# Kernel optimization log

Measured on AMD Instinct MI355X. Metric: run time of the kernel, lower is better.

Reference implementation:

```python
import jax, jax.numpy as jnp
import numpy as np

N_NODES = 50000
N_EDGES = 400000
DIMS = [128, 1024, 512, 256, 64, 1]  # ConvGraphNet layer widths


def setup_inputs() -> dict:
    key = jax.random.key(0)
    ks = jax.random.split(key, 2 + 2 * 5)
    inp = {}
    inp["x"] = jax.random.normal(ks[0], (N_NODES, DIMS[0]), dtype=jnp.float32)
    inp["edge_index"] = jax.random.randint(ks[1], (2, N_EDGES), 0, N_NODES, dtype=jnp.int32)
    for i in range(5):
        fan_in, fan_out = DIMS[i], DIMS[i + 1]
        scale = (1.0 / np.sqrt(fan_in)).astype(np.float32)
        inp[f"W{i+1}"] = jax.random.normal(ks[2 + 2 * i], (fan_in, fan_out), dtype=jnp.float32) * scale
        inp[f"b{i+1}"] = jax.random.normal(ks[3 + 2 * i], (fan_out,), dtype=jnp.float32) * 0.01
    return inp


def _gcn_forward(x, edge_index, params):
    # PyG GCNConv: add self-loops, symmetric deg^{-1/2} normalization,
    # h = x @ W, out[dst] += norm * h[src], + bias. ReLU after each layer.
    src, dst = edge_index[0], edge_index[1]
    loop = jnp.arange(N_NODES, dtype=src.dtype)
    src_f = jnp.concatenate([src, loop])  # [E + N]
    dst_f = jnp.concatenate([dst, loop])
    deg = jax.ops.segment_sum(jnp.ones_like(src_f, dtype=x.dtype), dst_f, num_segments=N_NODES)
    dinv = jnp.where(deg > 0, jax.lax.rsqrt(jnp.maximum(deg, 1e-12)), 0.0).astype(x.dtype)
    norm = (dinv[src_f] * dinv[dst_f])[:, None]  # [E + N, 1]
    for W, b in params:
        h = x @ W                      # [N, F_out] dense GEMM (small)
        msg = h[src_f] * norm          # gather + scale  [E+N, F_out]
        agg = jax.ops.segment_sum(msg, dst_f, num_segments=N_NODES)  # scatter-add
        x = jax.nn.relu(agg + b)
    return x


def reference(x, edge_index, W1, b1, W2, b2, W3, b3, W4, b4, W5, b5):
    params = [(W1, b1), (W2, b2), (W3, b3), (W4, b4), (W5, b5)]
    return _gcn_forward(x, edge_index, params)
```

## Files before the change

kernel.cpp:

```cpp
#include <hip/hip_runtime.h>
#include <hip/hip_bf16.h>

#define N_NODES_DIM0 128

typedef unsigned short u16;
typedef unsigned int u32;
typedef __attribute__((ext_vector_type(8))) short short8;
typedef __attribute__((ext_vector_type(4))) float f32x4;

__device__ __forceinline__ float bf2f(u16 h) { return __uint_as_float((u32)h << 16); }
__device__ __forceinline__ u16 f2bf(float f) {
    u32 u = __float_as_uint(f);
    u32 r = (u + 0x7FFFu + ((u >> 16) & 1u)) >> 16;
    return (u16)r;
}

__device__ __forceinline__ void gl2lds16(const u16* g, u16* lds_base) {
    __builtin_amdgcn_global_load_lds(
        (const __attribute__((address_space(1))) u32*)g,
        (__attribute__((address_space(3))) u32*)lds_base, 16, 0, 0);
}


__global__ void hist_kernel(const int* __restrict__ dst, int* __restrict__ cnt, int e) {
    int i = blockIdx.x * blockDim.x + threadIdx.x;
    if (i < e) atomicAdd(&cnt[dst[i]], 1);
}

__global__ void alloc_kernel(const int* __restrict__ cnt, int* __restrict__ row_start,
                             float* __restrict__ dinv, int* __restrict__ cursor, int n) {
    int i = blockIdx.x * blockDim.x + threadIdx.x;
    int lane = threadIdx.x & 63;
    int v = (i < n) ? cnt[i] : 0;
    int s = v;
#pragma unroll
    for (int off = 1; off < 64; off <<= 1) {
        int x = __shfl_up(s, off, 64);
        if (lane >= off) s += x;
    }
    int total = __shfl(s, 63, 64);
    int base = 0;
    if (lane == 0) base = atomicAdd(cursor, total);
    base = __shfl(base, 0, 64);
    if (i < n) {
        row_start[i] = base + s - v;
        dinv[i] = rsqrtf((float)v + 1.0f);
    }
}

__global__ void fill_kernel(const int* __restrict__ src, const int* __restrict__ dst,
                            int* __restrict__ row_start, int* __restrict__ csr_src, int e) {
    int i = blockIdx.x * blockDim.x + threadIdx.x;
    if (i < e) {
        int d = dst[i];
        int pos = atomicAdd(&row_start[d], 1);
        csr_src[pos] = src[i];
    }
}

__global__ __launch_bounds__(256) void prep_kernel(
    const float* __restrict__ W0, const float* __restrict__ W1,
    const float* __restrict__ W2, const float* __restrict__ W3, u16* __restrict__ Wt,
    const float* __restrict__ x, const float* __restrict__ dinv,
    u16* __restrict__ Y, int N) {
    int bid = blockIdx.x;
    if (bid < 784) {
        __shared__ float tile[32][33];
        const float* W; u16* out; int K, F, kb, nb;
        if (bid < 128)      { W = W0; out = Wt;          K = 128;  F = 1024; kb = bid & 3;  nb = bid >> 2; }
        else if (bid < 640) { int l = bid - 128; W = W1; out = Wt + 131072; K = 1024; F = 512; kb = l & 31; nb = l >> 5; }
        else if (bid < 768) { int l = bid - 640; W = W2; out = Wt + 655360; K = 512;  F = 256; kb = l & 15; nb = l >> 4; }
        else                { int l = bid - 768; W = W3; out = Wt + 786432; K = 256;  F = 64;  kb = l & 7;  nb = l >> 3; }
        int k0 = kb * 32, n0 = nb * 32;
        int tx = threadIdx.x & 31, ty = threadIdx.x >> 5;
#pragma unroll
        for (int i = 0; i < 4; ++i) {
            int k = ty + i * 8;
            tile[k][tx] = W[(size_t)(k0 + k) * F + n0 + tx];
        }
        __syncthreads();
#pragma unroll
        for (int i = 0; i < 4; ++i) {
            int n = ty + i * 8;
            out[(size_t)(n0 + n) * K + k0 + tx] = f2bf(tile[tx][n]);
        }
    } else {
        int gid = (bid - 784) * 256 + threadIdx.x;
        int node = gid >> 5;
        int c4 = (gid & 31) * 4;
        if (node >= N) return;
        float dv = dinv[node];
        float4 v = *reinterpret_cast<const float4*>(x + (size_t)node * 128 + c4);
        ushort4 r;
        r.x = f2bf(dv * v.x); r.y = f2bf(dv * v.y);
        r.z = f2bf(dv * v.z); r.w = f2bf(dv * v.w);
        *reinterpret_cast<ushort4*>(Y + (size_t)node * 128 + c4) = r;
    }
}

__device__ __forceinline__ void add8v(float* acc, short8 v) {
#pragma unroll
    for (int w = 0; w < 8; ++w) acc[w] += bf2f((u16)v[w]);
}
__device__ __forceinline__ void add16p(float* acc, const u16* p) {
    short8 a = *reinterpret_cast<const short8*>(p);
    short8 b = *reinterpret_cast<const short8*>(p + 8);
    add8v(acc, a); add8v(acc + 8, b);
}

__device__ __forceinline__ void gather_sum16(float* acc, const u16* __restrict__ base,
                                             const int* __restrict__ csr_src,
                                             int beg, int end, int stride, int ch) {
    int e = beg;
    int nfull = (end - beg) >> 3;
    if (nfull > 0) {
        int i0 = csr_src[e],     i1 = csr_src[e + 1], i2 = csr_src[e + 2], i3 = csr_src[e + 3];
        int i4 = csr_src[e + 4], i5 = csr_src[e + 5], i6 = csr_src[e + 6], i7 = csr_src[e + 7];
        for (int b = 0; b < nfull; ++b) {
            const u16* p0 = base + (size_t)i0 * stride + ch;
            const u16* p1 = base + (size_t)i1 * stride + ch;
            const u16* p2 = base + (size_t)i2 * stride + ch;
            const u16* p3 = base + (size_t)i3 * stride + ch;
            const u16* p4 = base + (size_t)i4 * stride + ch;
            const u16* p5 = base + (size_t)i5 * stride + ch;
            const u16* p6 = base + (size_t)i6 * stride + ch;
            const u16* p7 = base + (size_t)i7 * stride + ch;
            short8 a0 = *reinterpret_cast<const short8*>(p0), b0 = *reinterpret_cast<const short8*>(p0 + 8);
            short8 a1 = *reinterpret_cast<const short8*>(p1), b1 = *reinterpret_cast<const short8*>(p1 + 8);
            short8 a2 = *reinterpret_cast<const short8*>(p2), b2 = *reinterpret_cast<const short8*>(p2 + 8);
            short8 a3 = *reinterpret_cast<const short8*>(p3), b3 = *reinterpret_cast<const short8*>(p3 + 8);
            short8 a4 = *reinterpret_cast<const short8*>(p4), b4 = *reinterpret_cast<const short8*>(p4 + 8);
            short8 a5 = *reinterpret_cast<const short8*>(p5), b5 = *reinterpret_cast<const short8*>(p5 + 8);
            short8 a6 = *reinterpret_cast<const short8*>(p6), b6 = *reinterpret_cast<const short8*>(p6 + 8);
            short8 a7 = *reinterpret_cast<const short8*>(p7), b7 = *reinterpret_cast<const short8*>(p7 + 8);
            e += 8;
            int ep = (e + 8 <= end) ? e : beg;
            i0 = csr_src[ep];     i1 = csr_src[ep + 1]; i2 = csr_src[ep + 2]; i3 = csr_src[ep + 3];
            i4 = csr_src[ep + 4]; i5 = csr_src[ep + 5]; i6 = csr_src[ep + 6]; i7 = csr_src[ep + 7];
            __builtin_amdgcn_sched_barrier(0);
            add8v(acc, a0); add8v(acc + 8, b0);
            add8v(acc, a1); add8v(acc + 8, b1);
            add8v(acc, a2); add8v(acc + 8, b2);
            add8v(acc, a3); add8v(acc + 8, b3);
            add8v(acc, a4); add8v(acc + 8, b4);
            add8v(acc, a5); add8v(acc + 8, b5);
            add8v(acc, a6); add8v(acc + 8, b6);
            add8v(acc, a7); add8v(acc + 8, b7);
        }
    }
    for (; e + 4 <= end; e += 4) {
        const u16* p0 = base + (size_t)csr_src[e]     * stride + ch;
        const u16* p1 = base + (size_t)csr_src[e + 1] * stride + ch;
        const u16* p2 = base + (size_t)csr_src[e + 2] * stride + ch;
        const u16* p3 = base + (size_t)csr_src[e + 3] * stride + ch;
        short8 a0 = *reinterpret_cast<const short8*>(p0), b0 = *reinterpret_cast<const short8*>(p0 + 8);
        short8 a1 = *reinterpret_cast<const short8*>(p1), b1 = *reinterpret_cast<const short8*>(p1 + 8);
        short8 a2 = *reinterpret_cast<const short8*>(p2), b2 = *reinterpret_cast<const short8*>(p2 + 8);
        short8 a3 = *reinterpret_cast<const short8*>(p3), b3 = *reinterpret_cast<const short8*>(p3 + 8);
        __builtin_amdgcn_sched_barrier(0);
        add8v(acc, a0); add8v(acc + 8, b0);
        add8v(acc, a1); add8v(acc + 8, b1);
        add8v(acc, a2); add8v(acc + 8, b2);
        add8v(acc, a3); add8v(acc + 8, b3);
    }
    for (; e < end; ++e) {
        const u16* p = base + (size_t)csr_src[e] * stride + ch;
        short8 a = *reinterpret_cast<const short8*>(p), b = *reinterpret_cast<const short8*>(p + 8);
        add8v(acc, a); add8v(acc + 8, b);
    }
}

__global__ __launch_bounds__(256, 4) void agg_pre_kernel(
        const int* __restrict__ row_end, const int* __restrict__ cnt,
        const int* __restrict__ csr_src,
        const u16* __restrict__ Y, const float* __restrict__ dinv,
        u16* __restrict__ Z, int N) {
    int gid = blockIdx.x * blockDim.x + threadIdx.x;
    int node = gid >> 3;
    int ch = (gid & 7) * 16;
    if (node >= N) return;
    float acc[16] = {};
    add16p(acc, Y + (size_t)node * 128 + ch);
    int end = row_end[node], beg = end - cnt[node];
    gather_sum16(acc, Y, csr_src, beg, end, 128, ch);
    float dv = dinv[node];
    short8 r0, r1;
#pragma unroll
    for (int w = 0; w < 8; ++w) {
        r0[w] = (short)f2bf(dv * acc[w]);
        r1[w] = (short)f2bf(dv * acc[8 + w]);
    }
    *reinterpret_cast<short8*>(Z + (size_t)node * 128 + ch) = r0;
    *reinterpret_cast<short8*>(Z + (size_t)node * 128 + ch + 8) = r1;
}

template <int BN, int TPB, int EPI>
__global__ __launch_bounds__(TPB) void gemm_mfma_kernel(
    const u16* __restrict__ X, const u16* __restrict__ Wt,
    const float* __restrict__ dinv, const float* __restrict__ bias,
    u16* __restrict__ Out, int N, int K, int F, int lgnx) {
    constexpr int BM = 128, BK = 64;
    constexpr int RA = (BM * 8) / TPB;
    constexpr int RB = (BN * 8) / TPB;
    constexpr int WAVES = TPB / 64;
    constexpr int WAVES_N = (BN >= 64) ? (BN / 64) : 1;
    constexpr int WAVES_M = WAVES / WAVES_N;
    constexpr int WM = BM / WAVES_M;
    constexpr int WN = BN / WAVES_N;
    constexpr int NI = WM / 16;
    constexpr int NJ = WN / 16;
    __shared__ u16 As[BM * BK];
    __shared__ u16 Bs[BN * BK];

    const int t = threadIdx.x;
    const int wave = t >> 6;
    const int lane = t & 63;
    const int m16 = lane & 15;
    const int quad = lane >> 4;

    const int id = blockIdx.x;
    const int wi = id & ((8 << lgnx) - 1);
    const int g  = id >> (3 + lgnx);
    const int rb = g * 8 + (wi & 7);
    const int cb = wi >> 3;
    const int row0 = rb * BM;
    const int col0 = cb * BN;
    if (row0 >= N) return;

    const int wm = (wave / WAVES_N) * WM;
    const int wn = (wave % WAVES_N) * WN;

    const u16* aSrc[RA];
    u16* aDst[RA];
#pragma unroll
    for (int rr = 0; rr < RA; ++rr) {
        int c = rr * TPB + t;
        int r = c >> 3;
        int q = (c ^ r) & 7;
        int grow = row0 + r;
        if (grow >= N) grow = 0;
        aSrc[rr] = X + (size_t)grow * K + q * 8;
        aDst[rr] = &As[(size_t)(rr * TPB + wave * 64) * 8];
    }
    const u16* bSrc[RB];
    u16* bDst[RB];
#pragma unroll
    for (int rr = 0; rr < RB; ++rr) {
        int c = rr * TPB + t;
        int r = c >> 3;
        int q = (c ^ r) & 7;
        bSrc[rr] = Wt + (size_t)(col0 + r) * K + q * 8;
        bDst[rr] = &Bs[(size_t)(rr * TPB + wave * 64) * 8];
    }

    u32 aOff[NI][2], bOff[NJ][2];
#pragma unroll
    for (int i = 0; i < NI; ++i)
#pragma unroll
        for (int h = 0; h < 2; ++h) {
            int row = wm + i * 16 + m16;
            int qg = h * 4 + quad;
            aOff[i][h] = (u32)(((row << 3) | ((qg ^ row) & 7)) * 16);
        }
#pragma unroll
    for (int j = 0; j < NJ; ++j)
#pragma unroll
        for (int h = 0; h < 2; ++h) {
            int row = wn + j * 16 + m16;
            int qg = h * 4 + quad;
            bOff[j][h] = (u32)(((row << 3) | ((qg ^ row) & 7)) * 16);
        }
    const char* AsB = reinterpret_cast<const char*>(As);
    const char* BsB = reinterpret_cast<const char*>(Bs);

    f32x4 acc[NI][NJ] = {};

    for (int k0 = 0; k0 < K; k0 += BK) {
#pragma unroll
        for (int rr = 0; rr < RA; ++rr) {
            gl2lds16(aSrc[rr], aDst[rr]);
            aSrc[rr] += BK;
        }
#pragma unroll
        for (int rr = 0; rr < RB; ++rr) {
            gl2lds16(bSrc[rr], bDst[rr]);
            bSrc[rr] += BK;
        }
        __syncthreads();

#pragma unroll
        for (int h = 0; h < 2; ++h) {
            short8 af[NI], bf[NJ];
#pragma unroll
            for (int i = 0; i < NI; ++i)
                af[i] = *reinterpret_cast<const short8*>(AsB + aOff[i][h]);
#pragma unroll
            for (int j = 0; j < NJ; ++j)
                bf[j] = *reinterpret_cast<const short8*>(BsB + bOff[j][h]);
#pragma unroll
            for (int i = 0; i < NI; ++i)
#pragma unroll
                for (int j = 0; j < NJ; ++j)
                    acc[i][j] = __builtin_amdgcn_mfma_f32_16x16x32_bf16(af[i], bf[j], acc[i][j], 0, 0, 0);
        }
        __syncthreads();
    }

#pragma unroll
    for (int i = 0; i < NI; ++i) {
#pragma unroll
        for (int r = 0; r < 4; ++r) {
            int grow = row0 + wm + i * 16 + quad * 4 + r;
            if (grow >= N) continue;
            float dv = (EPI == 0) ? dinv[grow] : 0.f;
#pragma unroll
            for (int j = 0; j < NJ; ++j) {
                int gcol = col0 + wn + j * 16 + m16;
                float v = acc[i][j][r];
                if (EPI == 0) v = dv * v;
                else          v = fmaxf(v + bias[gcol], 0.f);
                Out[(size_t)grow * F + gcol] = f2bf(v);
            }
        }
    }
}

__global__ __launch_bounds__(256, 4) void agg_post_kernel(
        const int* __restrict__ row_end, const int* __restrict__ cnt,
        const int* __restrict__ csr_src,
        const u16* __restrict__ Gc, const float* __restrict__ dinv,
        const float* __restrict__ bias, u16* __restrict__ XO,
        int N, int F, int lgG) {
    int gid = blockIdx.x * blockDim.x + threadIdx.x;
    int node = gid >> lgG;
    int ch = (gid & ((1 << lgG) - 1)) * 16;
    if (node >= N) return;
    float acc[16] = {};
    add16p(acc, Gc + (size_t)node * F + ch);
    int end = row_end[node], beg = end - cnt[node];
    gather_sum16(acc, Gc, csr_src, beg, end, F, ch);
    float dv = dinv[node];
    short8 r0, r1;
#pragma unroll
    for (int w = 0; w < 8; ++w) {
        r0[w] = (short)f2bf(fmaxf(fmaf(dv, acc[w], bias[ch + w]), 0.f));
        r1[w] = (short)f2bf(fmaxf(fmaf(dv, acc[8 + w], bias[ch + 8 + w]), 0.f));
    }
    *reinterpret_cast<short8*>(XO + (size_t)node * F + ch) = r0;
    *reinterpret_cast<short8*>(XO + (size_t)node * F + ch + 8) = r1;
}

__global__ __launch_bounds__(256, 4) void agg_post_l5_kernel(
        const int* __restrict__ row_end, const int* __restrict__ cnt,
        const int* __restrict__ csr_src,
        const u16* __restrict__ Gc, const float* __restrict__ dinv,
        const float* __restrict__ b4, const float* __restrict__ W5,
        float* __restrict__ g5, int N) {
    int gid = blockIdx.x * blockDim.x + threadIdx.x;
    int node = gid >> 2;
    int ch = (gid & 3) * 16;
    if (node >= N) return;
    float acc[16] = {};
    add16p(acc, Gc + (size_t)node * 64 + ch);
    int end = row_end[node], beg = end - cnt[node];
    gather_sum16(acc, Gc, csr_src, beg, end, 64, ch);
    float dv = dinv[node];
    float dot = 0.f;
#pragma unroll
    for (int w = 0; w < 16; ++w) {
        float v = fmaxf(fmaf(dv, acc[w], b4[ch + w]), 0.f);
        dot = fmaf(v, W5[ch + w], dot);
    }
#pragma unroll
    for (int off = 2; off > 0; off >>= 1) dot += __shfl_down(dot, off, 4);
    if ((gid & 3) == 0) g5[node] = dv * dot;
}

__global__ void agg5_kernel(const int* __restrict__ row_end, const int* __restrict__ cnt,
                            const int* __restrict__ csr_src,
                            const float* __restrict__ g5, const float* __restrict__ dinv,
                            const float* __restrict__ b5, float* __restrict__ out, int N) {
    int i = blockIdx.x * blockDim.x + threadIdx.x;
    if (i >= N) return;
    float acc = g5[i];
    int end = row_end[i], e = end - cnt[i];
    for (; e + 4 <= end; e += 4) {
        float a = g5[csr_src[e]];
        float b = g5[csr_src[e + 1]];
        float c = g5[csr_src[e + 2]];
        float d = g5[csr_src[e + 3]];
        acc += (a + b) + (c + d);
    }
    for (; e < end; ++e) acc += g5[csr_src[e]];
    out[i] = fmaxf(fmaf(dinv[i], acc, b5[0]), 0.f);
}


static inline size_t align_up(size_t x) { return (x + 255) & ~(size_t)255; }
static inline int round_up8(int x) { return (x + 7) & ~7; }

extern "C" void kernel_launch(void* const* d_in, const int* in_sizes, int n_in,
                              void* d_out, int out_size, void* d_ws, size_t ws_size,
                              hipStream_t stream) {
    const float* x  = (const float*)d_in[0];
    const int*   ei = (const int*)d_in[1];
    const int E = in_sizes[1] / 2;
    const int N = in_sizes[0] / N_NODES_DIM0;
    const int* src = ei;
    const int* dst = ei + E;

    const float* W[5] = {(const float*)d_in[2], (const float*)d_in[4], (const float*)d_in[6],
                         (const float*)d_in[8], (const float*)d_in[10]};
    const float* B[5] = {(const float*)d_in[3], (const float*)d_in[5], (const float*)d_in[7],
                         (const float*)d_in[9], (const float*)d_in[11]};

    const int Ks[4] = {128, 1024, 512, 256};
    const int Fs[4] = {1024, 512, 256, 64};

    char* w = (char*)d_ws;
    size_t off = 0;
    float* dinv    = (float*)(w + off); off += align_up((size_t)N * 4);
    float* g5      = (float*)(w + off); off += align_up((size_t)N * 4);
    int*   cnt     = (int*)(w + off);   off += align_up((size_t)(N + 1) * 4);
    int*   rstart  = (int*)(w + off);   off += align_up((size_t)N * 4);
    int*   csr_src = (int*)(w + off);   off += align_up((size_t)E * 4);
    u16* WtBase = (u16*)(w + off);
    u16* Wt[4];
    {
        size_t cum = 0;
        for (int l = 0; l < 4; ++l) {
            Wt[l] = WtBase + cum;
            cum += (size_t)Ks[l] * Fs[l];
        }
        off += align_up(cum * 2);
    }
    char* REG = w + off;               off += align_up((size_t)N * 512 * 2);
    u16* Y  = (u16*)REG;
    u16* Z  = (u16*)(REG + align_up((size_t)N * 128 * 2));
    u16* Gc = (u16*)REG;
    u16* XA = (u16*)(w + off);         off += align_up((size_t)N * 1024 * 2);
    u16* XB = (u16*)(w + off);         off += align_up((size_t)N * 512 * 2);
    (void)ws_size;

    hipMemsetAsync(cnt, 0, (size_t)(N + 1) * 4, stream);
    hist_kernel<<<(E + 255) / 256, 256, 0, stream>>>(dst, cnt, E);
    alloc_kernel<<<(N + 255) / 256, 256, 0, stream>>>(cnt, rstart, dinv, &cnt[N], N);
    fill_kernel<<<(E + 255) / 256, 256, 0, stream>>>(src, dst, rstart, csr_src, E);

    {
        int scale_blocks = (N * 32 + 255) / 256;
        prep_kernel<<<784 + scale_blocks, 256, 0, stream>>>(
            W[0], W[1], W[2], W[3], WtBase, x, dinv, Y, N);
    }

    const int ny = (N + 127) / 128;
    const int ny8 = round_up8(ny);

    agg_pre_kernel<<<(N * 8 + 255) / 256, 256, 0, stream>>>(rstart, cnt, csr_src, Y, dinv, Z, N);
    {
        gemm_mfma_kernel<256, 512, 1><<<ny8 * 4, 512, 0, stream>>>(Z, Wt[0], dinv, B[0], XA,
                                                                   N, 128, 1024, 2);
    }

    u16* Xin[3]  = {XA, XB, XA};
    u16* Xout[3] = {XB, XA, nullptr};
    for (int l = 1; l < 4; ++l) {
        const int K = Ks[l], F = Fs[l];
        if (F >= 256) {
            int nx = F / 256;
            int lgnx = (nx == 2) ? 1 : 0;
            gemm_mfma_kernel<256, 512, 0><<<ny8 * nx, 512, 0, stream>>>(
                Xin[l - 1], Wt[l], dinv, B[l], Gc, N, K, F, lgnx);
        } else {
            gemm_mfma_kernel<64, 256, 0><<<ny8, 256, 0, stream>>>(
                Xin[l - 1], Wt[l], dinv, B[l], Gc, N, K, F, 0);
        }
        if (l < 3) {
            int lgG = (F == 512) ? 5 : 4;
            long long tot = (long long)N << lgG;
            agg_post_kernel<<<(unsigned)((tot + 255) / 256), 256, 0, stream>>>(
                rstart, cnt, csr_src, Gc, dinv, B[l], Xout[l - 1], N, F, lgG);
        } else {
            long long tot = (long long)N << 2;
            agg_post_l5_kernel<<<(unsigned)((tot + 255) / 256), 256, 0, stream>>>(
                rstart, cnt, csr_src, Gc, dinv, B[3], W[4], g5, N);
        }
    }

    agg5_kernel<<<(N + 255) / 256, 256, 0, stream>>>(rstart, cnt, csr_src, g5, dinv, B[4],
                                                     (float*)d_out, N);
}
```

Measured before the change: 414.9 us.

## Fuse layer-2 aggregation with layer-3 GEMM using LDS-resident aggregated tile

Replaces the separate layer-2 aggregation kernel and layer-3 GEMM with one kernel. Each block gathers the 512-wide neighbor sums for 64 nodes, applies bias, ReLU and bf16 rounding into a swizzled LDS tile, then multiplies that tile by W3 with MFMA while streaming W3 chunks into LDS. This removes the round trip of the 512-wide activation through global memory. In exchange it uses a large LDS footprint (about 80KB), which lowers occupancy, and the GEMM phase is small per block and re-reads W3 in every block.

```diff
diff --git a/kernel.cpp b/kernel.cpp
--- a/kernel.cpp
+++ b/kernel.cpp
@@ -170,6 +170,37 @@
     }
 }
 
+__device__ __forceinline__ void gather32(float* acc, const u16* __restrict__ base,
+                                         const int* __restrict__ csr_src,
+                                         int beg, int end, int ch) {
+    int e = beg;
+    for (; e + 4 <= end; e += 4) {
+        const u16* p0 = base + (size_t)csr_src[e]     * 512 + ch;
+        const u16* p1 = base + (size_t)csr_src[e + 1] * 512 + ch;
+        const u16* p2 = base + (size_t)csr_src[e + 2] * 512 + ch;
+        const u16* p3 = base + (size_t)csr_src[e + 3] * 512 + ch;
+        short8 a0 = *reinterpret_cast<const short8*>(p0),      b0 = *reinterpret_cast<const short8*>(p0 + 8);
+        short8 c0 = *reinterpret_cast<const short8*>(p0 + 16), d0 = *reinterpret_cast<const short8*>(p0 + 24);
+        short8 a1 = *reinterpret_cast<const short8*>(p1),      b1 = *reinterpret_cast<const short8*>(p1 + 8);
+        short8 c1 = *reinterpret_cast<const short8*>(p1 + 16), d1 = *reinterpret_cast<const short8*>(p1 + 24);
+        short8 a2 = *reinterpret_cast<const short8*>(p2),      b2 = *reinterpret_cast<const short8*>(p2 + 8);
+        short8 c2 = *reinterpret_cast<const short8*>(p2 + 16), d2 = *reinterpret_cast<const short8*>(p2 + 24);
+        short8 a3 = *reinterpret_cast<const short8*>(p3),      b3 = *reinterpret_cast<const short8*>(p3 + 8);
+        short8 c3 = *reinterpret_cast<const short8*>(p3 + 16), d3 = *reinterpret_cast<const short8*>(p3 + 24);
+        __builtin_amdgcn_sched_barrier(0);
+        add8v(acc, a0); add8v(acc + 8, b0); add8v(acc + 16, c0); add8v(acc + 24, d0);
+        add8v(acc, a1); add8v(acc + 8, b1); add8v(acc + 16, c1); add8v(acc + 24, d1);
+        add8v(acc, a2); add8v(acc + 8, b2); add8v(acc + 16, c2); add8v(acc + 24, d2);
+        add8v(acc, a3); add8v(acc + 8, b3); add8v(acc + 16, c3); add8v(acc + 24, d3);
+    }
+    for (; e < end; ++e) {
+        const u16* p = base + (size_t)csr_src[e] * 512 + ch;
+        short8 a = *reinterpret_cast<const short8*>(p),      b = *reinterpret_cast<const short8*>(p + 8);
+        short8 c = *reinterpret_cast<const short8*>(p + 16), d = *reinterpret_cast<const short8*>(p + 24);
+        add8v(acc, a); add8v(acc + 8, b); add8v(acc + 16, c); add8v(acc + 24, d);
+    }
+}
+
 __global__ __launch_bounds__(256, 4) void agg_pre_kernel(
         const int* __restrict__ row_end, const int* __restrict__ cnt,
         const int* __restrict__ csr_src,
@@ -325,6 +356,127 @@
     }
 }
 
+__global__ __launch_bounds__(512, 4) void fused_agg_gemm_kernel(
+        const int* __restrict__ row_end, const int* __restrict__ cnt,
+        const int* __restrict__ csr_src, const u16* __restrict__ Gc,
+        const float* __restrict__ dinv, const float* __restrict__ bias,
+        const u16* __restrict__ Wt3, u16* __restrict__ Out, int N) {
+    __shared__ u16 Z[64 * 512];
+    __shared__ u16 Wb[128 * 64];
+
+    const int t = threadIdx.x;
+    const int id = blockIdx.x;
+    const int rb = (id >> 3) * 8 + (id & 7);
+    const int row0 = rb * 64;
+    if (row0 >= N) return;
+
+    {
+        const int nl = t >> 3;
+        const int sub = t & 7;
+        const int node = row0 + nl;
+        int end = 0, beg = 0;
+        float dv = 0.f;
+        if (node < N) {
+            end = row_end[node];
+            beg = end - cnt[node];
+            dv = dinv[node];
+        }
+#pragma unroll
+        for (int p = 0; p < 2; ++p) {
+            const int ch = sub * 64 + p * 32;
+            float acc[32] = {};
+            if (node < N) {
+                const u16* sp = Gc + (size_t)node * 512 + ch;
+                add8v(acc, *reinterpret_cast<const short8*>(sp));
+                add8v(acc + 8, *reinterpret_cast<const short8*>(sp + 8));
+                add8v(acc + 16, *reinterpret_cast<const short8*>(sp + 16));
+                add8v(acc + 24, *reinterpret_cast<const short8*>(sp + 24));
+                gather32(acc, Gc, csr_src, beg, end, ch);
+            }
+#pragma unroll
+            for (int cq = 0; cq < 4; ++cq) {
+                int kc = (ch >> 3) + cq;
+                short8 r;
+#pragma unroll
+                for (int w = 0; w < 8; ++w)
+                    r[w] = (short)f2bf(fmaxf(fmaf(dv, acc[cq * 8 + w], bias[ch + cq * 8 + w]), 0.f));
+                int slot = nl * 64 + ((kc & ~7) | ((kc ^ nl) & 7));
+                *reinterpret_cast<short8*>(&Z[slot * 8]) = r;
+            }
+        }
+    }
+    __syncthreads();
+
+    const int wave = t >> 6;
+    const int lane = t & 63;
+    const int m16 = lane & 15;
+    const int quad = lane >> 4;
+    const int wm = (wave >> 1) * 16;
+    const int wn = (wave & 1) * 64;
+
+    const int arow = wm + m16;
+    const char* ZB = reinterpret_cast<const char*>(Z);
+    const char* WbB = reinterpret_cast<const char*>(Wb);
+
+    u32 aOffh[2];
+#pragma unroll
+    for (int h = 0; h < 2; ++h)
+        aOffh[h] = (u32)(arow * 1024 + (((h * 4 + quad) ^ (arow & 7)) * 16));
+    u32 bOff[4][2];
+#pragma unroll
+    for (int j = 0; j < 4; ++j)
+#pragma unroll
+        for (int h = 0; h < 2; ++h) {
+            int rowb = wn + j * 16 + m16;
+            bOff[j][h] = (u32)(((rowb << 3) | (((h * 4 + quad) ^ rowb) & 7)) * 16);
+        }
+    u32 bR[2], bQ[2];
+    u16* bDst[2];
+#pragma unroll
+    for (int rr = 0; rr < 2; ++rr) {
+        int c = rr * 512 + t;
+        bR[rr] = (u32)(c >> 3);
+        bQ[rr] = (u32)((c ^ (c >> 3)) & 7);
+        bDst[rr] = &Wb[(size_t)(rr * 512 + wave * 64) * 8];
+    }
+
+#pragma unroll
+    for (int cbp = 0; cbp < 2; ++cbp) {
+        f32x4 acc[4] = {};
+        for (int k0 = 0; k0 < 512; k0 += 64) {
+#pragma unroll
+            for (int rr = 0; rr < 2; ++rr) {
+                const u16* src = Wt3 + (size_t)(cbp * 128 + bR[rr]) * 512 + k0 + bQ[rr] * 8;
+                gl2lds16(src, bDst[rr]);
+            }
+            __syncthreads();
+#pragma unroll
+            for (int h = 0; h < 2; ++h) {
+                short8 af = *reinterpret_cast<const short8*>(ZB + aOffh[h] + k0 * 2);
+                short8 bf[4];
+#pragma unroll
+                for (int j = 0; j < 4; ++j)
+                    bf[j] = *reinterpret_cast<const short8*>(WbB + bOff[j][h]);
+#pragma unroll
+                for (int j = 0; j < 4; ++j)
+                    acc[j] = __builtin_amdgcn_mfma_f32_16x16x32_bf16(af, bf[j], acc[j], 0, 0, 0);
+            }
+            __syncthreads();
+        }
+#pragma unroll
+        for (int r = 0; r < 4; ++r) {
+            int grow = row0 + wm + quad * 4 + r;
+            if (grow >= N) continue;
+            float dv = dinv[grow];
+#pragma unroll
+            for (int j = 0; j < 4; ++j) {
+                int gcol = cbp * 128 + wn + j * 16 + m16;
+                Out[(size_t)grow * 256 + gcol] = f2bf(dv * acc[j][r]);
+            }
+        }
+    }
+}
+
 __global__ __launch_bounds__(256, 4) void agg_post_kernel(
         const int* __restrict__ row_end, const int* __restrict__ cnt,
         const int* __restrict__ csr_src,
@@ -457,35 +609,26 @@
     const int ny8 = round_up8(ny);
 
     agg_pre_kernel<<<(N * 8 + 255) / 256, 256, 0, stream>>>(rstart, cnt, csr_src, Y, dinv, Z, N);
+    gemm_mfma_kernel<256, 512, 1><<<ny8 * 4, 512, 0, stream>>>(Z, Wt[0], dinv, B[0], XA,
+                                                               N, 128, 1024, 2);
+
+    gemm_mfma_kernel<256, 512, 0><<<ny8 * 2, 512, 0, stream>>>(XA, Wt[1], dinv, B[1], Gc,
+                                                               N, 1024, 512, 1);
+
     {
-        gemm_mfma_kernel<256, 512, 1><<<ny8 * 4, 512, 0, stream>>>(Z, Wt[0], dinv, B[0], XA,
-                                                                   N, 128, 1024, 2);
-    }
-
-    u16* Xin[3]  = {XA, XB, XA};
-    u16* Xout[3] = {XB, XA, nullptr};
-    for (int l = 1; l < 4; ++l) {
-        const int K = Ks[l], F = Fs[l];
-        if (F >= 256) {
-            int nx = F / 256;
-            int lgnx = (nx == 2) ? 1 : 0;
-            gemm_mfma_kernel<256, 512, 0><<<ny8 * nx, 512, 0, stream>>>(
-                Xin[l - 1], Wt[l], dinv, B[l], Gc, N, K, F, lgnx);
-        } else {
-            gemm_mfma_kernel<64, 256, 0><<<ny8, 256, 0, stream>>>(
-                Xin[l - 1], Wt[l], dinv, B[l], Gc, N, K, F, 0);
-        }
-        if (l < 3) {
-            int lgG = (F == 512) ? 5 : 4;
-            long long tot = (long long)N << lgG;
-            agg_post_kernel<<<(unsigned)((tot + 255) / 256), 256, 0, stream>>>(
-                rstart, cnt, csr_src, Gc, dinv, B[l], Xout[l - 1], N, F, lgG);
-        } else {
-            long long tot = (long long)N << 2;
-            agg_post_l5_kernel<<<(unsigned)((tot + 255) / 256), 256, 0, stream>>>(
-                rstart, cnt, csr_src, Gc, dinv, B[3], W[4], g5, N);
-        }
-    }
+        int ny64 = round_up8((N + 63) / 64);
+        fused_agg_gemm_kernel<<<ny64, 512, 0, stream>>>(rstart, cnt, csr_src, Gc, dinv, B[1],
+                                                        Wt[2], XB, N);
+    }
+
+    agg_post_kernel<<<(N * 16 + 255) / 256, 256, 0, stream>>>(rstart, cnt, csr_src, XB, dinv,
+                                                              B[2], XA, N, 256, 4);
+
+    gemm_mfma_kernel<64, 256, 0><<<ny8, 256, 0, stream>>>(XA, Wt[3], dinv, B[3], Gc,
+                                                          N, 256, 64, 0);
+
+    agg_post_l5_kernel<<<(unsigned)(((long long)N * 4 + 255) / 256), 256, 0, stream>>>(
+        rstart, cnt, csr_src, Gc, dinv, B[3], W[4], g5, N);
 
     agg5_kernel<<<(N + 255) / 256, 256, 0, stream>>>(rstart, cnt, csr_src, g5, dinv, B[4],
                                                      (float*)d_out, N);
```

Result: slower. 484.9 us (+16.9%).

## Split layers into row halves and co-schedule aggregation with GEMM in fused kernels

Applied to the files above, without the earlier changes.

Each layer's node range is split in two halves. The first-half aggregation runs alone. A fused kernel then runs the first-half GEMM blocks alongside the second-half aggregation blocks, and a separate GEMM finishes the second half. This overlaps memory-bound gather work with MFMA-bound GEMM work to fill idle CUs between dependent stages. It adds more launches, uses 512-thread aggregation blocks in the fused kernels, and requires careful buffer aliasing (Gc256 placed inside XA) to avoid read/write conflicts.

```diff
diff --git a/kernel.cpp b/kernel.cpp
--- a/kernel.cpp
+++ b/kernel.cpp
@@ -170,35 +170,50 @@
     }
 }
 
-__global__ __launch_bounds__(256, 4) void agg_pre_kernel(
-        const int* __restrict__ row_end, const int* __restrict__ cnt,
-        const int* __restrict__ csr_src,
-        const u16* __restrict__ Y, const float* __restrict__ dinv,
-        u16* __restrict__ Z, int N) {
-    int gid = blockIdx.x * blockDim.x + threadIdx.x;
-    int node = gid >> 3;
-    int ch = (gid & 7) * 16;
-    if (node >= N) return;
+template <int TPB, int MODE>
+__device__ __forceinline__ void agg_dev(
+        int bid, int t, const int* __restrict__ row_end, const int* __restrict__ cnt,
+        const int* __restrict__ csr_src, const u16* Gin, const float* __restrict__ dinv,
+        const float* __restrict__ bias, u16* XO, int nodeBeg, int nodeEnd, int F, int lgG) {
+    int gid = bid * TPB + t;
+    int node = nodeBeg + (gid >> lgG);
+    int ch = (gid & ((1 << lgG) - 1)) * 16;
+    if (node >= nodeEnd) return;
     float acc[16] = {};
-    add16p(acc, Y + (size_t)node * 128 + ch);
+    add16p(acc, Gin + (size_t)node * F + ch);
     int end = row_end[node], beg = end - cnt[node];
-    gather_sum16(acc, Y, csr_src, beg, end, 128, ch);
+    gather_sum16(acc, Gin, csr_src, beg, end, F, ch);
     float dv = dinv[node];
     short8 r0, r1;
 #pragma unroll
     for (int w = 0; w < 8; ++w) {
-        r0[w] = (short)f2bf(dv * acc[w]);
-        r1[w] = (short)f2bf(dv * acc[8 + w]);
-    }
-    *reinterpret_cast<short8*>(Z + (size_t)node * 128 + ch) = r0;
-    *reinterpret_cast<short8*>(Z + (size_t)node * 128 + ch + 8) = r1;
+        if (MODE == 0) {
+            r0[w] = (short)f2bf(dv * acc[w]);
+            r1[w] = (short)f2bf(dv * acc[8 + w]);
+        } else {
+            r0[w] = (short)f2bf(fmaxf(fmaf(dv, acc[w], bias[ch + w]), 0.f));
+            r1[w] = (short)f2bf(fmaxf(fmaf(dv, acc[8 + w], bias[ch + 8 + w]), 0.f));
+        }
+    }
+    *reinterpret_cast<short8*>(XO + (size_t)node * F + ch) = r0;
+    *reinterpret_cast<short8*>(XO + (size_t)node * F + ch + 8) = r1;
+}
+
+template <int TPB, int MODE>
+__global__ __launch_bounds__(TPB, 4) void agg_kernel(
+        const int* __restrict__ row_end, const int* __restrict__ cnt,
+        const int* __restrict__ csr_src, const u16* Gin, const float* __restrict__ dinv,
+        const float* __restrict__ bias, u16* XO, int nodeBeg, int nodeEnd, int F, int lgG) {
+    agg_dev<TPB, MODE>(blockIdx.x, threadIdx.x, row_end, cnt, csr_src, Gin, dinv, bias, XO,
+                       nodeBeg, nodeEnd, F, lgG);
 }
 
 template <int BN, int TPB, int EPI>
-__global__ __launch_bounds__(TPB) void gemm_mfma_kernel(
-    const u16* __restrict__ X, const u16* __restrict__ Wt,
+__device__ __forceinline__ void gemm_dev(
+    u16* As, u16* Bs, int bid, int t,
+    const u16* X, const u16* __restrict__ Wt,
     const float* __restrict__ dinv, const float* __restrict__ bias,
-    u16* __restrict__ Out, int N, int K, int F, int lgnx) {
+    u16* Out, int rowBeg, int rowEnd, int N, int K, int F, int lgnx) {
     constexpr int BM = 128, BK = 64;
     constexpr int RA = (BM * 8) / TPB;
     constexpr int RB = (BN * 8) / TPB;
@@ -209,23 +224,19 @@
     constexpr int WN = BN / WAVES_N;
     constexpr int NI = WM / 16;
     constexpr int NJ = WN / 16;
-    __shared__ u16 As[BM * BK];
-    __shared__ u16 Bs[BN * BK];
-
-    const int t = threadIdx.x;
+
     const int wave = t >> 6;
     const int lane = t & 63;
     const int m16 = lane & 15;
     const int quad = lane >> 4;
 
-    const int id = blockIdx.x;
-    const int wi = id & ((8 << lgnx) - 1);
-    const int g  = id >> (3 + lgnx);
+    const int wi = bid & ((8 << lgnx) - 1);
+    const int g  = bid >> (3 + lgnx);
     const int rb = g * 8 + (wi & 7);
     const int cb = wi >> 3;
-    const int row0 = rb * BM;
+    const int row0 = rowBeg + rb * BM;
     const int col0 = cb * BN;
-    if (row0 >= N) return;
+    if (row0 >= rowEnd) return;
 
     const int wm = (wave / WAVES_N) * WM;
     const int wn = (wave % WAVES_N) * WN;
@@ -325,29 +336,64 @@
     }
 }
 
-__global__ __launch_bounds__(256, 4) void agg_post_kernel(
+template <int BN, int TPB, int EPI>
+__global__ __launch_bounds__(TPB) void gemm_mfma_kernel(
+    const u16* X, const u16* __restrict__ Wt,
+    const float* __restrict__ dinv, const float* __restrict__ bias,
+    u16* Out, int rowBeg, int rowEnd, int N, int K, int F, int lgnx) {
+    __shared__ u16 As[128 * 64];
+    __shared__ u16 Bs[BN * 64];
+    gemm_dev<BN, TPB, EPI>(As, Bs, blockIdx.x, threadIdx.x, X, Wt, dinv, bias, Out,
+                           rowBeg, rowEnd, N, K, F, lgnx);
+}
+
+
+__global__ __launch_bounds__(512) void fused_aggpre_gemm1_kernel(
         const int* __restrict__ row_end, const int* __restrict__ cnt,
-        const int* __restrict__ csr_src,
-        const u16* __restrict__ Gc, const float* __restrict__ dinv,
-        const float* __restrict__ bias, u16* __restrict__ XO,
-        int N, int F, int lgG) {
-    int gid = blockIdx.x * blockDim.x + threadIdx.x;
-    int node = gid >> lgG;
-    int ch = (gid & ((1 << lgG) - 1)) * 16;
-    if (node >= N) return;
-    float acc[16] = {};
-    add16p(acc, Gc + (size_t)node * F + ch);
-    int end = row_end[node], beg = end - cnt[node];
-    gather_sum16(acc, Gc, csr_src, beg, end, F, ch);
-    float dv = dinv[node];
-    short8 r0, r1;
-#pragma unroll
-    for (int w = 0; w < 8; ++w) {
-        r0[w] = (short)f2bf(fmaxf(fmaf(dv, acc[w], bias[ch + w]), 0.f));
-        r1[w] = (short)f2bf(fmaxf(fmaf(dv, acc[8 + w], bias[ch + 8 + w]), 0.f));
-    }
-    *reinterpret_cast<short8*>(XO + (size_t)node * F + ch) = r0;
-    *reinterpret_cast<short8*>(XO + (size_t)node * F + ch + 8) = r1;
+        const int* __restrict__ csr_src, const u16* Y, const float* __restrict__ dinv,
+        u16* Z, const u16* __restrict__ Wt0, const float* __restrict__ b0, u16* XA,
+        int nG, int M0, int N) {
+    __shared__ u16 As[128 * 64];
+    __shared__ u16 Bs[256 * 64];
+    int bid = blockIdx.x;
+    if (bid < nG)
+        gemm_dev<256, 512, 1>(As, Bs, bid, threadIdx.x, Z, Wt0, dinv, b0, XA,
+                              0, M0, N, 128, 1024, 2);
+    else
+        agg_dev<512, 0>(bid - nG, threadIdx.x, row_end, cnt, csr_src, Y, dinv, nullptr, Z,
+                        M0, N, 128, 3);
+}
+
+__global__ __launch_bounds__(512) void fused_agg2_gemm3_kernel(
+        const int* __restrict__ row_end, const int* __restrict__ cnt,
+        const int* __restrict__ csr_src, const u16* Gc512, const float* __restrict__ dinv,
+        const float* __restrict__ b1, u16* XB, const u16* __restrict__ Wt2, u16* Gc256,
+        int nG, int M0, int N) {
+    __shared__ u16 As[128 * 64];
+    __shared__ u16 Bs[256 * 64];
+    int bid = blockIdx.x;
+    if (bid < nG)
+        gemm_dev<256, 512, 0>(As, Bs, bid, threadIdx.x, XB, Wt2, dinv, b1, Gc256,
+                              0, M0, N, 512, 256, 0);
+    else
+        agg_dev<512, 1>(bid - nG, threadIdx.x, row_end, cnt, csr_src, Gc512, dinv, b1, XB,
+                        M0, N, 512, 5);
+}
+
+__global__ __launch_bounds__(512) void fused_agg3_gemm4_kernel(
+        const int* __restrict__ row_end, const int* __restrict__ cnt,
+        const int* __restrict__ csr_src, const u16* Gc256, const float* __restrict__ dinv,
+        const float* __restrict__ b2, u16* XAlow, const u16* __restrict__ Wt3,
+        const float* __restrict__ b3, u16* Gc64, int nG, int M0, int N) {
+    __shared__ u16 As[128 * 64];
+    __shared__ u16 Bs[64 * 64];
+    int bid = blockIdx.x;
+    if (bid < nG)
+        gemm_dev<64, 512, 0>(As, Bs, bid, threadIdx.x, XAlow, Wt3, dinv, b3, Gc64,
+                             0, M0, N, 256, 64, 0);
+    else
+        agg_dev<512, 1>(bid - nG, threadIdx.x, row_end, cnt, csr_src, Gc256, dinv, b2, XAlow,
+                        M0, N, 256, 4);
 }
 
 __global__ __launch_bounds__(256, 4) void agg_post_l5_kernel(
@@ -440,6 +486,7 @@
     u16* Gc = (u16*)REG;
     u16* XA = (u16*)(w + off);         off += align_up((size_t)N * 1024 * 2);
     u16* XB = (u16*)(w + off);         off += align_up((size_t)N * 512 * 2);
+    u16* Gc256 = XA + (size_t)N * 512;
     (void)ws_size;
 
     hipMemsetAsync(cnt, 0, (size_t)(N + 1) * 4, stream);
@@ -453,39 +500,55 @@
             W[0], W[1], W[2], W[3], WtBase, x, dinv, Y, N);
     }
 
-    const int ny = (N + 127) / 128;
-    const int ny8 = round_up8(ny);
-
-    agg_pre_kernel<<<(N * 8 + 255) / 256, 256, 0, stream>>>(rstart, cnt, csr_src, Y, dinv, Z, N);
+    const int ny  = (N + 127) / 128;
+    const int nyh = (ny + 1) / 2;
+    const int M0  = nyh * 128;
+    const int ny8  = round_up8(ny);
+    const int ny8h = round_up8(nyh);
+    const int ny8r = round_up8(ny - nyh);
+    const int h1nodes = (N > M0) ? (N - M0) : 0;
+
+    agg_kernel<256, 0><<<(M0 * 8 + 255) / 256, 256, 0, stream>>>(
+        rstart, cnt, csr_src, Y, dinv, nullptr, Z, 0, M0 < N ? M0 : N, 128, 3);
     {
-        gemm_mfma_kernel<256, 512, 1><<<ny8 * 4, 512, 0, stream>>>(Z, Wt[0], dinv, B[0], XA,
-                                                                   N, 128, 1024, 2);
-    }
-
-    u16* Xin[3]  = {XA, XB, XA};
-    u16* Xout[3] = {XB, XA, nullptr};
-    for (int l = 1; l < 4; ++l) {
-        const int K = Ks[l], F = Fs[l];
-        if (F >= 256) {
-            int nx = F / 256;
-            int lgnx = (nx == 2) ? 1 : 0;
-            gemm_mfma_kernel<256, 512, 0><<<ny8 * nx, 512, 0, stream>>>(
-                Xin[l - 1], Wt[l], dinv, B[l], Gc, N, K, F, lgnx);
-        } else {
-            gemm_mfma_kernel<64, 256, 0><<<ny8, 256, 0, stream>>>(
-                Xin[l - 1], Wt[l], dinv, B[l], Gc, N, K, F, 0);
-        }
-        if (l < 3) {
-            int lgG = (F == 512) ? 5 : 4;
-            long long tot = (long long)N << lgG;
-            agg_post_kernel<<<(unsigned)((tot + 255) / 256), 256, 0, stream>>>(
-                rstart, cnt, csr_src, Gc, dinv, B[l], Xout[l - 1], N, F, lgG);
-        } else {
-            long long tot = (long long)N << 2;
-            agg_post_l5_kernel<<<(unsigned)((tot + 255) / 256), 256, 0, stream>>>(
-                rstart, cnt, csr_src, Gc, dinv, B[3], W[4], g5, N);
-        }
-    }
+        int nG = ny8h * 4;
+        int nA = (h1nodes * 8 + 511) / 512;
+        fused_aggpre_gemm1_kernel<<<nG + nA, 512, 0, stream>>>(
+            rstart, cnt, csr_src, Y, dinv, Z, Wt[0], B[0], XA, nG, M0, N);
+    }
+    if (ny > nyh)
+        gemm_mfma_kernel<256, 512, 1><<<ny8r * 4, 512, 0, stream>>>(
+            Z, Wt[0], dinv, B[0], XA, M0, N, N, 128, 1024, 2);
+
+    gemm_mfma_kernel<256, 512, 0><<<ny8 * 2, 512, 0, stream>>>(
+        XA, Wt[1], dinv, B[1], Gc, 0, N, N, 1024, 512, 1);
+
+    agg_kernel<256, 1><<<(M0 * 32 + 255) / 256, 256, 0, stream>>>(
+        rstart, cnt, csr_src, Gc, dinv, B[1], XB, 0, M0 < N ? M0 : N, 512, 5);
+    {
+        int nG = ny8h;
+        int nA = (h1nodes * 32 + 511) / 512;
+        fused_agg2_gemm3_kernel<<<nG + nA, 512, 0, stream>>>(
+            rstart, cnt, csr_src, Gc, dinv, B[1], XB, Wt[2], Gc256, nG, M0, N);
+    }
+    if (ny > nyh)
+        gemm_mfma_kernel<256, 512, 0><<<ny8r, 512, 0, stream>>>(
+            XB, Wt[2], dinv, B[1], Gc256, M0, N, N, 512, 256, 0);
+
+    agg_kernel<256, 1><<<(M0 * 16 + 255) / 256, 256, 0, stream>>>(
+        rstart, cnt, csr_src, Gc256, dinv, B[2], XA, 0, M0 < N ? M0 : N, 256, 4);
+    {
+        int nG = ny8h;
+        int nA = (h1nodes * 16 + 511) / 512;
+        fused_agg3_gemm4_kernel<<<nG + nA, 512, 0, stream>>>(
+            rstart, cnt, csr_src, Gc256, dinv, B[2], XA, Wt[3], B[3], Gc, nG, M0, N);
+    }
+    if (ny > nyh)
+        gemm_mfma_kernel<64, 512, 0><<<ny8r, 512, 0, stream>>>(
+            XA, Wt[3], dinv, B[3], Gc, M0, N, N, 256, 64, 0);
+
+    agg_post_l5_kernel<<<(unsigned)(((long long)N * 4 + 255) / 256), 256, 0, stream>>>(
+        rstart, cnt, csr_src, Gc, dinv, B[3], W[4], g5, N);
 
     agg5_kernel<<<(N + 255) / 256, 256, 0, stream>>>(rstart, cnt, csr_src, g5, dinv, B[4],
                                                      (float*)d_out, N);
```

Result: slower. 442.8 us (+6.7%).
